# Optimization experiments

Hardware: AMD Instinct MI355X
Metric: run time of the kernel (lower is better)

## Reference

```python
import jax, jax.numpy as jnp
import numpy as np
import math

B, T, C, H = 8, 1024, 768, 12
HD = C // H  # 64


def setup_inputs() -> dict:
    key = jax.random.key(0)
    k1, k2, k3 = jax.random.split(key, 3)
    x = jax.random.normal(k1, (B, T, C), dtype=jnp.float32)
    W_attn = jax.random.normal(k2, (C, 3 * C), dtype=jnp.float32) * 0.02
    b_attn = jnp.zeros((3 * C,), dtype=jnp.float32)
    W_proj = jax.random.normal(k3, (C, C), dtype=jnp.float32) * (0.02 / math.sqrt(2 * 12))
    b_proj = jnp.zeros((C,), dtype=jnp.float32)
    return {"x": x, "W_attn": W_attn, "b_attn": b_attn, "W_proj": W_proj, "b_proj": b_proj}


def reference(x, W_attn, b_attn, W_proj, b_proj):
    Bx, Tx, Cx = x.shape
    qkv = x @ W_attn + b_attn                        # [B,T,3C]
    # faithful to original: reshape to (B,T,H,3*HD) then split last axis
    qkv = qkv.reshape(Bx, Tx, H, 3 * HD).transpose(0, 2, 1, 3)  # [B,H,T,3*HD]
    q, k, v = jnp.split(qkv, 3, axis=-1)             # each [B,H,T,HD]
    att = jnp.einsum('bhqd,bhkd->bhqk', q, k) / math.sqrt(HD)
    causal = jnp.tril(jnp.ones((Tx, Tx), dtype=bool))
    att = jnp.where(causal, att, -jnp.inf)
    att = jax.nn.softmax(att, axis=-1)
    y = jnp.einsum('bhqk,bhkd->bhqd', att, v)        # [B,H,T,HD]
    y = y.transpose(0, 2, 1, 3).reshape(Bx, Tx, Cx)  # [B,T,C]
    return y @ W_proj + b_proj
```

## Files before the change

### kernel.cpp

```cpp
#include <hip/hip_runtime.h>
#include <hip/hip_bf16.h>


#define TDIM 1024
#define CDIM 768
#define NDIM 2304

typedef __attribute__((ext_vector_type(8))) short bf16x8;
typedef __attribute__((ext_vector_type(8))) unsigned short u16x8;
typedef __attribute__((ext_vector_type(4))) float f32x4;

__device__ __forceinline__ unsigned short f2bf(float f) {
    unsigned int u;
    __builtin_memcpy(&u, &f, 4);
    u += 0x7FFFu + ((u >> 16) & 1u);
    return (unsigned short)(u >> 16);
}

__device__ __forceinline__ void async_copy16(void* lds, const void* g) {
    __builtin_amdgcn_global_load_lds(
        (const __attribute__((address_space(1))) void*)g,
        (__attribute__((address_space(3))) void*)lds, 16, 0, 0);
}

__global__ __launch_bounds__(256) void precast(
    const float* __restrict__ x, unsigned short* __restrict__ xb,
    const float* __restrict__ Wa, unsigned short* __restrict__ Wta,
    const float* __restrict__ Wp, unsigned short* __restrict__ Wtp)
{
    __shared__ float tile[32][33];
    int bid = blockIdx.x;
    const int tid = threadIdx.x;

    if (bid < 6144) {
        const size_t i = ((size_t)bid * 256 + tid) * 4;
        float4 v = *(const float4*)&x[i];
        ushort4 s;
        s.x = f2bf(v.x); s.y = f2bf(v.y); s.z = f2bf(v.z); s.w = f2bf(v.w);
        *(ushort4*)&xb[i] = s;
        return;
    }
    bid -= 6144;
    const float* W;
    unsigned short* Wt;
    int N, bx, by;
    if (bid < 1728) {
        W = Wa; Wt = Wta; N = NDIM; bx = bid % 72; by = bid / 72;
    } else {
        bid -= 1728;
        W = Wp; Wt = Wtp; N = CDIM; bx = bid % 24; by = bid / 24;
    }
    const int n0 = bx * 32;
    const int k0 = by * 32;
    const int tx = tid & 31;
    const int ty = tid >> 5;
#pragma unroll
    for (int i = 0; i < 4; ++i)
        tile[ty + i * 8][tx] = W[(size_t)(k0 + ty + i * 8) * N + n0 + tx];
    __syncthreads();
#pragma unroll
    for (int i = 0; i < 4; ++i)
        Wt[(size_t)(n0 + ty + i * 8) * CDIM + k0 + tx] = f2bf(tile[tx][ty + i * 8]);
}

__global__ __launch_bounds__(512, 4) void qkv_mfma(
    const unsigned short* __restrict__ xb, const unsigned short* __restrict__ Wt,
    const float* __restrict__ bias,
    unsigned short* __restrict__ Q, unsigned short* __restrict__ Kd,
    unsigned short* __restrict__ Vt)
{
    const int wg = ((int)blockIdx.x & 7) * 72 + ((int)blockIdx.x >> 3);
    const int bx = wg % 9;
    const int by = wg / 9;
    const int n0 = bx * 256;
    const int m0 = by * 128;
    const int tid = threadIdx.x;
    const int lane = tid & 63;
    const int w = tid >> 6;
    const int wm = w >> 2;
    const int wn = w & 3;
    const int lm = lane & 15;
    const int lq = lane >> 4;

    __shared__ __align__(16) unsigned short lds[36864];

    float bb[4];
#pragma unroll
    for (int ni = 0; ni < 4; ++ni) bb[ni] = bias[n0 + wn * 64 + ni * 16 + lm];

    f32x4 acc[4][4] = {};

    const int eo = lq ^ ((lm >> 1) & 3);
    int aoffc[4], boffc[4];
#pragma unroll
    for (int mi = 0; mi < 4; ++mi)
        aoffc[mi] = (wm * 64 + mi * 16 + lm) * 32 + eo * 8;
#pragma unroll
    for (int ni = 0; ni < 4; ++ni)
        boffc[ni] = 4096 + (wn * 64 + ni * 16 + lm) * 32 + eo * 8;

    const int rowA = tid >> 2;
    const int ccA = (tid & 3) ^ ((rowA >> 1) & 3);
    const int srcA = rowA * CDIM + ccA * 8;
    int srcB[2];
#pragma unroll
    for (int j = 0; j < 2; ++j) {
        const int lin = j * 512 + tid;
        const int rowB = lin >> 2;
        const int ccB = (lin & 3) ^ ((rowB >> 1) & 3);
        srcB[j] = rowB * CDIM + ccB * 8;
    }
    const unsigned short* xbb = xb + (size_t)m0 * CDIM;
    const unsigned short* Wtb = Wt + (size_t)n0 * CDIM;

#define STAGE(p, kt)                                                            \
    do {                                                                        \
        async_copy16(&lds[(p) * 12288 + w * 512], &xbb[srcA + (kt) * 32]);      \
        _Pragma("unroll")                                                       \
        for (int j = 0; j < 2; ++j)                                             \
            async_copy16(&lds[(p) * 12288 + 4096 + j * 4096 + w * 512],         \
                         &Wtb[srcB[j] + (kt) * 32]);                            \
    } while (0)

#define TILE(p, ktn)                                                            \
    do {                                                                        \
        STAGE((p + 2) % 3, ktn);                                                \
        bf16x8 a[4], b[4];                                                      \
        _Pragma("unroll")                                                       \
        for (int mi = 0; mi < 4; ++mi)                                          \
            a[mi] = *(const bf16x8*)&lds[(p) * 12288 + aoffc[mi]];              \
        _Pragma("unroll")                                                       \
        for (int ni = 0; ni < 4; ++ni)                                          \
            b[ni] = *(const bf16x8*)&lds[(p) * 12288 + boffc[ni]];              \
        __builtin_amdgcn_s_setprio(1);                                          \
        _Pragma("unroll")                                                       \
        for (int mi = 0; mi < 4; ++mi)                                          \
            _Pragma("unroll")                                                   \
            for (int ni = 0; ni < 4; ++ni)                                      \
                acc[mi][ni] = __builtin_amdgcn_mfma_f32_16x16x32_bf16(          \
                    a[mi], b[ni], acc[mi][ni], 0, 0, 0);                        \
        __builtin_amdgcn_s_setprio(0);                                          \
        asm volatile("s_waitcnt vmcnt(3)" ::: "memory");                        \
        __builtin_amdgcn_s_barrier();                                           \
    } while (0)

    STAGE(0, 0);
    STAGE(1, 1);
    asm volatile("s_waitcnt vmcnt(3)" ::: "memory");
    __builtin_amdgcn_s_barrier();

#pragma unroll 1
    for (int it = 0; it < 8; ++it) {
        const int k2 = (3 * it + 2 < 24) ? 3 * it + 2 : 23;
        const int k3 = (3 * it + 3 < 24) ? 3 * it + 3 : 23;
        const int k4 = (3 * it + 4 < 24) ? 3 * it + 4 : 23;
        TILE(0, k2);
        TILE(1, k3);
        TILE(2, k4);
    }

#undef STAGE
#undef TILE

    asm volatile("s_waitcnt vmcnt(0)" ::: "memory");
    __builtin_amdgcn_s_barrier();

    const int ga = bx * 4 + wn;
    const int which = ga % 3;
    const int h = ga / 3;

    if (which == 2) {
#pragma unroll
        for (int ni = 0; ni < 4; ++ni) {
            const int d = ni * 16 + lm;
#pragma unroll
            for (int mi = 0; mi < 4; ++mi) {
                const int gm0 = m0 + wm * 64 + mi * 16 + lq * 4;
                const int bidx = gm0 >> 10;
                const int t0 = gm0 & 1023;
                ushort4 sv;
                sv.x = f2bf(acc[mi][ni][0] + bb[ni]);
                sv.y = f2bf(acc[mi][ni][1] + bb[ni]);
                sv.z = f2bf(acc[mi][ni][2] + bb[ni]);
                sv.w = f2bf(acc[mi][ni][3] + bb[ni]);
                *(ushort4*)&Vt[(((size_t)bidx * 12 + h) * 64 + d) * TDIM + t0] = sv;
            }
        }
    } else {
        unsigned short* dst = (which == 0) ? Q : Kd;
        unsigned short* Es = &lds[w * 1152];
        const int erow = lane >> 2;
        const int ecol = lane & 3;
#pragma unroll
        for (int mi = 0; mi < 4; ++mi) {
#pragma unroll
            for (int r = 0; r < 4; ++r)
#pragma unroll
                for (int ni = 0; ni < 4; ++ni)
                    Es[(lq * 4 + r) * 72 + ni * 16 + lm] = f2bf(acc[mi][ni][r] + bb[ni]);
            const int t = m0 + wm * 64 + mi * 16 + erow;
            const int bidx = t >> 10;
            const int tt = t & 1023;
            unsigned short* drow = &dst[(((size_t)bidx * 12 + h) * TDIM + tt) * 64];
            u16x8 v0 = *(const u16x8*)&Es[erow * 72 + ecol * 16];
            u16x8 v1 = *(const u16x8*)&Es[erow * 72 + ecol * 16 + 8];
            *(u16x8*)&drow[ecol * 16] = v0;
            *(u16x8*)&drow[ecol * 16 + 8] = v1;
        }
    }
}

#define ATTN_TILE(aq, q0t, qt_t, l_p, o, ksb, vsb) do {                         \
    const bool diag_ = (kt == (qt_t));                                          \
    float pf[4][4];                                                             \
    _Pragma("unroll")                                                           \
    for (int nt = 0; nt < 4; ++nt) {                                            \
        f32x4 s = {};                                                           \
        _Pragma("unroll")                                                       \
        for (int kc = 0; kc < 2; ++kc) {                                        \
            bf16x8 bfrag = *(const bf16x8*)&(ksb)[(nt * 16 + lm) * 64 + cofs[kc]]; \
            s = __builtin_amdgcn_mfma_f32_16x16x32_bf16(aq[kc], bfrag, s, 0, 0, 0); \
        }                                                                       \
        const int keyg = kbase + nt * 16 + lm;                                  \
        _Pragma("unroll")                                                       \
        for (int r = 0; r < 4; ++r) {                                           \
            float p = __builtin_amdgcn_exp2f(s[r] * SC);                        \
            if (diag_) {                                                        \
                const int qg = (q0t) + w * 16 + lq * 4 + r;                     \
                if (keyg > qg) p = 0.f;                                         \
            }                                                                   \
            pf[nt][r] = p;                                                      \
        }                                                                       \
    }                                                                           \
    _Pragma("unroll")                                                           \
    for (int r = 0; r < 4; ++r) {                                               \
        l_p[r] += pf[0][r] + pf[1][r] + pf[2][r] + pf[3][r];                    \
        _Pragma("unroll")                                                       \
        for (int nt = 0; nt < 4; ++nt)                                          \
            Ps[w][lq * 4 + r][nt * 16 + lm] = f2bf(pf[nt][r]);                  \
    }                                                                           \
    {                                                                           \
        bf16x8 ap[2];                                                           \
        _Pragma("unroll")                                                       \
        for (int kc = 0; kc < 2; ++kc)                                          \
            ap[kc] = *(const bf16x8*)&Ps[w][lm][kc * 32 + lq * 8];              \
        _Pragma("unroll")                                                       \
        for (int nt = 0; nt < 4; ++nt) {                                        \
            _Pragma("unroll")                                                   \
            for (int kc = 0; kc < 2; ++kc) {                                    \
                bf16x8 bv = *(const bf16x8*)&(vsb)[(nt * 16 + lm) * 64 + cofs[kc]]; \
                o[nt] = __builtin_amdgcn_mfma_f32_16x16x32_bf16(ap[kc], bv, o[nt], 0, 0, 0); \
            }                                                                   \
        }                                                                       \
    }                                                                           \
} while (0)

#define ATTN_EPI(q0t, l_p, o) do {                                              \
    _Pragma("unroll")                                                           \
    for (int r = 0; r < 4; ++r) {                                               \
        float l = l_p[r];                                                       \
        _Pragma("unroll")                                                       \
        for (int off = 1; off < 16; off <<= 1) l += __shfl_xor(l, off);         \
        const float inv = 1.0f / l;                                             \
        const int qg = (q0t) + w * 16 + lq * 4 + r;                             \
        _Pragma("unroll")                                                       \
        for (int nt = 0; nt < 4; ++nt)                                          \
            Yb[(size_t)qg * 64 + nt * 16 + lm] = f2bf(o[nt][r] * inv);          \
    }                                                                           \
} while (0)

__global__ __launch_bounds__(256) void attn_mfma(
    const unsigned short* __restrict__ Q, const unsigned short* __restrict__ K,
    const unsigned short* __restrict__ Vt, unsigned short* __restrict__ Y)
{
    const int pi = blockIdx.x;
    const int bh = blockIdx.y;
    const int qtA = pi, qtB = 15 - pi;
    const int q0A = qtA * 64, q0B = qtB * 64;
    const int tid = threadIdx.x;
    const int lane = tid & 63;
    const int w = tid >> 6;
    const int lm = lane & 15;
    const int lq = lane >> 4;

    __shared__ __align__(16) unsigned short Ks2[2][4096];
    __shared__ __align__(16) unsigned short Vts2[2][4096];
    __shared__ __align__(16) unsigned short Ps[4][16][72];

    const unsigned short* Qb = Q + (size_t)bh * TDIM * 64;
    const unsigned short* Kb = K + (size_t)bh * TDIM * 64;
    const unsigned short* Vtb = Vt + (size_t)bh * 64 * TDIM;
    unsigned short* Yb = Y + (size_t)bh * TDIM * 64;

    bf16x8 aqA[2], aqB[2];
#pragma unroll
    for (int kc = 0; kc < 2; ++kc) {
        aqA[kc] = *(const bf16x8*)&Qb[(size_t)(q0A + w * 16 + lm) * 64 + kc * 32 + lq * 8];
        aqB[kc] = *(const bf16x8*)&Qb[(size_t)(q0B + w * 16 + lm) * 64 + kc * 32 + lq * 8];
    }

    int dstO[2], srcK[2], srcV[2];
#pragma unroll
    for (int it = 0; it < 2; ++it) {
        const int idx = it * 256 + tid;
        const int row = idx >> 3;
        const int cc = (idx & 7) ^ (row & 7);
        dstO[it] = idx * 8;
        srcK[it] = row * 64 + cc * 8;
        srcV[it] = row * TDIM + cc * 8;
    }
    int cofs[2];
#pragma unroll
    for (int kc = 0; kc < 2; ++kc)
        cofs[kc] = (((kc * 4 + lq) ^ (lm & 7)) * 8);

#define AST(bf, kb)                                                             \
    do {                                                                        \
        _Pragma("unroll")                                                       \
        for (int it = 0; it < 2; ++it) {                                        \
            async_copy16(&Ks2[bf][dstO[it]], &Kb[(size_t)(kb) * 64 + srcK[it]]); \
            async_copy16(&Vts2[bf][dstO[it]], &Vtb[(size_t)(kb) + srcV[it]]);   \
        }                                                                       \
    } while (0)

    float lA[4] = {}, lB[4] = {};
    f32x4 oA[4] = {}, oB[4] = {};

    const float SC = 0.125f * 1.44269504f;
    const int nktA = qtA + 1;
    const int nktB = qtB + 1;

    int buf = 0;
    AST(0, 0);
    asm volatile("s_waitcnt vmcnt(0)" ::: "memory");
    __builtin_amdgcn_s_barrier();

    for (int kt = 0; kt < nktB; ++kt) {
        const int kbase = kt * 64;
        if (kt + 1 < nktB) AST(buf ^ 1, kbase + 64);

        ATTN_TILE(aqB, q0B, qtB, lB, oB, Ks2[buf], Vts2[buf]);
        if (kt < nktA) ATTN_TILE(aqA, q0A, qtA, lA, oA, Ks2[buf], Vts2[buf]);

        asm volatile("s_waitcnt vmcnt(0)" ::: "memory");
        __builtin_amdgcn_s_barrier();
        buf ^= 1;
    }

#undef AST

    ATTN_EPI(q0A, lA, oA);
    ATTN_EPI(q0B, lB, oB);
}

__global__ __launch_bounds__(256, 3) void proj_mfma(
    const unsigned short* __restrict__ Y, const unsigned short* __restrict__ Wt,
    const float* __restrict__ bias, float* __restrict__ out)
{
    const int wg = ((int)blockIdx.x & 7) * 48 + ((int)blockIdx.x >> 3);
    const int bx = wg % 6;
    const int by = wg / 6;
    const int n0 = bx * 128;
    const int m0 = by * 128;
    const int tid = threadIdx.x;
    const int lane = tid & 63;
    const int w = tid >> 6;
    const int wm = w >> 1;
    const int wn = w & 1;
    const int lm = lane & 15;
    const int lq = lane >> 4;

    __shared__ __align__(16) unsigned short lds[24576];

    float bb[4];
#pragma unroll
    for (int ni = 0; ni < 4; ++ni) bb[ni] = bias[n0 + wn * 64 + ni * 16 + lm];

    f32x4 acc[4][4] = {};

    const int eo = lq ^ ((lm >> 1) & 3);
    int aoffc[4], boffc[4];
#pragma unroll
    for (int mi = 0; mi < 4; ++mi)
        aoffc[mi] = (wm * 64 + mi * 16 + lm) * 32 + eo * 8;
#pragma unroll
    for (int ni = 0; ni < 4; ++ni)
        boffc[ni] = 4096 + (wn * 64 + ni * 16 + lm) * 32 + eo * 8;

    size_t srcA[2];
    int srcB[2];
#pragma unroll
    for (int j = 0; j < 2; ++j) {
        const int lin = j * 256 + tid;
        const int row = lin >> 2;
        const int cc = (lin & 3) ^ ((row >> 1) & 3);
        const int m = m0 + row;
        srcA[j] = (size_t)(m >> 10) * 786432 + (size_t)(m & 1023) * 64 + cc * 8;
        srcB[j] = row * CDIM + cc * 8;
    }
    const unsigned short* Wtb = Wt + (size_t)n0 * CDIM;

#define PSTAGE(p, kt)                                                           \
    do {                                                                        \
        const int hof = ((kt) >> 1) * 65536 + ((kt) & 1) * 32;                  \
        _Pragma("unroll")                                                       \
        for (int j = 0; j < 2; ++j)                                             \
            async_copy16(&lds[(p) * 8192 + (j * 256 + tid) * 8],                \
                         &Y[srcA[j] + hof]);                                    \
        _Pragma("unroll")                                                       \
        for (int j = 0; j < 2; ++j)                                             \
            async_copy16(&lds[(p) * 8192 + 4096 + (j * 256 + tid) * 8],         \
                         &Wtb[srcB[j] + (kt) * 32]);                            \
    } while (0)

#define PTILE(p, ktn)                                                           \
    do {                                                                        \
        PSTAGE((p + 2) % 3, ktn);                                               \
        bf16x8 a[4], b[4];                                                      \
        _Pragma("unroll")                                                       \
        for (int mi = 0; mi < 4; ++mi)                                          \
            a[mi] = *(const bf16x8*)&lds[(p) * 8192 + aoffc[mi]];               \
        _Pragma("unroll")                                                       \
        for (int ni = 0; ni < 4; ++ni)                                          \
            b[ni] = *(const bf16x8*)&lds[(p) * 8192 + boffc[ni]];               \
        __builtin_amdgcn_s_setprio(1);                                          \
        _Pragma("unroll")                                                       \
        for (int mi = 0; mi < 4; ++mi)                                          \
            _Pragma("unroll")                                                   \
            for (int ni = 0; ni < 4; ++ni)                                      \
                acc[mi][ni] = __builtin_amdgcn_mfma_f32_16x16x32_bf16(          \
                    a[mi], b[ni], acc[mi][ni], 0, 0, 0);                        \
        __builtin_amdgcn_s_setprio(0);                                          \
        asm volatile("s_waitcnt vmcnt(4)" ::: "memory");                        \
        __builtin_amdgcn_s_barrier();                                           \
    } while (0)

    PSTAGE(0, 0);
    PSTAGE(1, 1);
    asm volatile("s_waitcnt vmcnt(4)" ::: "memory");
    __builtin_amdgcn_s_barrier();

#pragma unroll 1
    for (int it = 0; it < 8; ++it) {
        const int k2 = (3 * it + 2 < 24) ? 3 * it + 2 : 23;
        const int k3 = (3 * it + 3 < 24) ? 3 * it + 3 : 23;
        const int k4 = (3 * it + 4 < 24) ? 3 * it + 4 : 23;
        PTILE(0, k2);
        PTILE(1, k3);
        PTILE(2, k4);
    }

#undef PSTAGE
#undef PTILE

    asm volatile("s_waitcnt vmcnt(0)" ::: "memory");

#pragma unroll
    for (int ni = 0; ni < 4; ++ni) {
        const int gn = n0 + wn * 64 + ni * 16 + lm;
#pragma unroll
        for (int mi = 0; mi < 4; ++mi) {
#pragma unroll
            for (int r = 0; r < 4; ++r) {
                const int gm = m0 + wm * 64 + mi * 16 + lq * 4 + r;
                out[(size_t)gm * CDIM + gn] = acc[mi][ni][r] + bb[ni];
            }
        }
    }
}

extern "C" void kernel_launch(void* const* d_in, const int* in_sizes, int n_in,
                              void* d_out, int out_size, void* d_ws, size_t ws_size,
                              hipStream_t stream) {
    const float* x      = (const float*)d_in[0];
    const float* W_attn = (const float*)d_in[1];
    const float* b_attn = (const float*)d_in[2];
    const float* W_proj = (const float*)d_in[3];
    const float* b_proj = (const float*)d_in[4];
    float* out = (float*)d_out;

    const size_t per = (size_t)8 * 12 * 1024 * 64;
    unsigned short* Q   = (unsigned short*)d_ws;
    unsigned short* K   = Q + per;
    unsigned short* Vt  = K + per;
    unsigned short* xb  = Vt + per;
    unsigned short* Wta = xb + (size_t)8192 * CDIM;
    unsigned short* Wtp = Wta + (size_t)NDIM * CDIM;

    precast<<<dim3(8448), 256, 0, stream>>>(x, xb, W_attn, Wta, W_proj, Wtp);

    qkv_mfma<<<dim3(576), 512, 0, stream>>>(xb, Wta, b_attn, Q, K, Vt);
    attn_mfma<<<dim3(8, 96), 256, 0, stream>>>(Q, K, Vt, Q);
    proj_mfma<<<dim3(384), 256, 0, stream>>>(Q, Wtp, b_proj, out);
}
```

Measured before the change: 182.1 us.

## Load QKV GEMM weight fragments directly from global into registers, bypassing LDS

The QKV projection GEMM no longer stages the weight (B) tile through shared memory. Each wave now reads its B fragments straight from global memory into registers, and only the activation (A) tile stays in a triple-buffered LDS pipeline. This cuts LDS use per block from 72KB to 24KB, which can raise occupancy and removes the LDS reads for B. In exchange, B loads are issued just before the MFMAs, so their global/L2 latency is exposed; the two waves sharing a column read the same B twice; and the reads are strided across rows.

Result: slower. 223.9 us (+22.9%).

```diff
diff --git a/kernel.cpp b/kernel.cpp
--- a/kernel.cpp
+++ b/kernel.cpp
@@ -82,7 +82,7 @@
     const int lm = lane & 15;
     const int lq = lane >> 4;
 
-    __shared__ __align__(16) unsigned short lds[36864];
+    __shared__ __align__(16) unsigned short lds[12288];
 
     float bb[4];
 #pragma unroll
@@ -91,47 +91,31 @@
     f32x4 acc[4][4] = {};
 
     const int eo = lq ^ ((lm >> 1) & 3);
-    int aoffc[4], boffc[4];
+    int aoffc[4];
 #pragma unroll
     for (int mi = 0; mi < 4; ++mi)
         aoffc[mi] = (wm * 64 + mi * 16 + lm) * 32 + eo * 8;
-#pragma unroll
-    for (int ni = 0; ni < 4; ++ni)
-        boffc[ni] = 4096 + (wn * 64 + ni * 16 + lm) * 32 + eo * 8;
 
     const int rowA = tid >> 2;
     const int ccA = (tid & 3) ^ ((rowA >> 1) & 3);
     const int srcA = rowA * CDIM + ccA * 8;
-    int srcB[2];
-#pragma unroll
-    for (int j = 0; j < 2; ++j) {
-        const int lin = j * 512 + tid;
-        const int rowB = lin >> 2;
-        const int ccB = (lin & 3) ^ ((rowB >> 1) & 3);
-        srcB[j] = rowB * CDIM + ccB * 8;
-    }
     const unsigned short* xbb = xb + (size_t)m0 * CDIM;
-    const unsigned short* Wtb = Wt + (size_t)n0 * CDIM;
-
-#define STAGE(p, kt)                                                            \
+
+    const unsigned short* Bp = Wt + (size_t)(n0 + wn * 64 + lm) * CDIM + lq * 8;
+
+#define STAGE(p, kt) async_copy16(&lds[(p) * 4096 + tid * 8], &xbb[srcA + (kt) * 32])
+
+#define TILE(p, ktc, kts)                                                       \
     do {                                                                        \
-        async_copy16(&lds[(p) * 12288 + w * 512], &xbb[srcA + (kt) * 32]);      \
-        _Pragma("unroll")                                                       \
-        for (int j = 0; j < 2; ++j)                                             \
-            async_copy16(&lds[(p) * 12288 + 4096 + j * 4096 + w * 512],         \
-                         &Wtb[srcB[j] + (kt) * 32]);                            \
-    } while (0)
-
-#define TILE(p, ktn)                                                            \
-    do {                                                                        \
-        STAGE((p + 2) % 3, ktn);                                                \
-        bf16x8 a[4], b[4];                                                      \
+        bf16x8 b[4];                                                            \
+        _Pragma("unroll")                                                       \
+        for (int ni = 0; ni < 4; ++ni)                                          \
+            b[ni] = *(const bf16x8*)(Bp + ni * 16 * CDIM + (ktc) * 32);         \
+        STAGE((p + 2) % 3, kts);                                                \
+        bf16x8 a[4];                                                            \
         _Pragma("unroll")                                                       \
         for (int mi = 0; mi < 4; ++mi)                                          \
-            a[mi] = *(const bf16x8*)&lds[(p) * 12288 + aoffc[mi]];              \
-        _Pragma("unroll")                                                       \
-        for (int ni = 0; ni < 4; ++ni)                                          \
-            b[ni] = *(const bf16x8*)&lds[(p) * 12288 + boffc[ni]];              \
+            a[mi] = *(const bf16x8*)&lds[(p) * 4096 + aoffc[mi]];               \
         __builtin_amdgcn_s_setprio(1);                                          \
         _Pragma("unroll")                                                       \
         for (int mi = 0; mi < 4; ++mi)                                          \
@@ -140,23 +124,21 @@
                 acc[mi][ni] = __builtin_amdgcn_mfma_f32_16x16x32_bf16(          \
                     a[mi], b[ni], acc[mi][ni], 0, 0, 0);                        \
         __builtin_amdgcn_s_setprio(0);                                          \
-        asm volatile("s_waitcnt vmcnt(3)" ::: "memory");                        \
+        asm volatile("s_waitcnt vmcnt(1)" ::: "memory");                        \
         __builtin_amdgcn_s_barrier();                                           \
     } while (0)
 
     STAGE(0, 0);
     STAGE(1, 1);
-    asm volatile("s_waitcnt vmcnt(3)" ::: "memory");
+    asm volatile("s_waitcnt vmcnt(1)" ::: "memory");
     __builtin_amdgcn_s_barrier();
 
 #pragma unroll 1
     for (int it = 0; it < 8; ++it) {
-        const int k2 = (3 * it + 2 < 24) ? 3 * it + 2 : 23;
-        const int k3 = (3 * it + 3 < 24) ? 3 * it + 3 : 23;
-        const int k4 = (3 * it + 4 < 24) ? 3 * it + 4 : 23;
-        TILE(0, k2);
-        TILE(1, k3);
-        TILE(2, k4);
+        const int t0 = 3 * it;
+        TILE(0, t0,     (t0 + 2 < 24) ? t0 + 2 : 23);
+        TILE(1, t0 + 1, (t0 + 3 < 24) ? t0 + 3 : 23);
+        TILE(2, t0 + 2, (t0 + 4 < 24) ? t0 + 4 : 23);
     }
 
 #undef STAGE
```

## Interleave QK/softmax/PV phases of paired tiles and peel diagonal iterations

Applied to the files above, without the earlier changes.

Splits the attention tile into separate QK, softmax and PV stages and interleaves them across the two query tiles A and B, each with its own P buffer in LDS, so the MFMAs of one tile can overlap the exp and LDS work of the other. The key loop is also split into phases with compile-time flags, so causal masking code runs only on the diagonal iterations and the per-iteration `kt < nktA` check is removed. In exchange it doubles the P scratch in LDS and keeps more live score registers, which may add register pressure and lower occupancy.

After: 189.6 us. 4.1% more time.

```diff
diff --git a/kernel.cpp b/kernel.cpp
--- a/kernel.cpp
+++ b/kernel.cpp
@@ -210,9 +210,7 @@
     }
 }
 
-#define ATTN_TILE(aq, q0t, qt_t, l_p, o, ksb, vsb) do {                         \
-    const bool diag_ = (kt == (qt_t));                                          \
-    float pf[4][4];                                                             \
+#define QK_PART(sf, aq, ksb) do {                                               \
     _Pragma("unroll")                                                           \
     for (int nt = 0; nt < 4; ++nt) {                                            \
         f32x4 s = {};                                                           \
@@ -221,11 +219,19 @@
             bf16x8 bfrag = *(const bf16x8*)&(ksb)[(nt * 16 + lm) * 64 + cofs[kc]]; \
             s = __builtin_amdgcn_mfma_f32_16x16x32_bf16(aq[kc], bfrag, s, 0, 0, 0); \
         }                                                                       \
-        const int keyg = kbase + nt * 16 + lm;                                  \
+        sf[nt] = s;                                                             \
+    }                                                                           \
+} while (0)
+
+#define SM_PART(sf, l_p, ps, DIAG, q0t) do {                                    \
+    float pf[4][4];                                                             \
+    _Pragma("unroll")                                                           \
+    for (int nt = 0; nt < 4; ++nt) {                                            \
         _Pragma("unroll")                                                       \
         for (int r = 0; r < 4; ++r) {                                           \
-            float p = __builtin_amdgcn_exp2f(s[r] * SC);                        \
-            if (diag_) {                                                        \
+            float p = __builtin_amdgcn_exp2f(sf[nt][r] * SC);                   \
+            if (DIAG) {                                                         \
+                const int keyg = kbase + nt * 16 + lm;                          \
                 const int qg = (q0t) + w * 16 + lq * 4 + r;                     \
                 if (keyg > qg) p = 0.f;                                         \
             }                                                                   \
@@ -237,20 +243,21 @@
         l_p[r] += pf[0][r] + pf[1][r] + pf[2][r] + pf[3][r];                    \
         _Pragma("unroll")                                                       \
         for (int nt = 0; nt < 4; ++nt)                                          \
-            Ps[w][lq * 4 + r][nt * 16 + lm] = f2bf(pf[nt][r]);                  \
+            (ps)[(lq * 4 + r) * 72 + nt * 16 + lm] = f2bf(pf[nt][r]);           \
     }                                                                           \
-    {                                                                           \
-        bf16x8 ap[2];                                                           \
-        _Pragma("unroll")                                                       \
-        for (int kc = 0; kc < 2; ++kc)                                          \
-            ap[kc] = *(const bf16x8*)&Ps[w][lm][kc * 32 + lq * 8];              \
-        _Pragma("unroll")                                                       \
-        for (int nt = 0; nt < 4; ++nt) {                                        \
-            _Pragma("unroll")                                                   \
-            for (int kc = 0; kc < 2; ++kc) {                                    \
-                bf16x8 bv = *(const bf16x8*)&(vsb)[(nt * 16 + lm) * 64 + cofs[kc]]; \
-                o[nt] = __builtin_amdgcn_mfma_f32_16x16x32_bf16(ap[kc], bv, o[nt], 0, 0, 0); \
-            }                                                                   \
+} while (0)
+
+#define PV_PART(o, ps, vsb) do {                                                \
+    bf16x8 ap[2];                                                               \
+    _Pragma("unroll")                                                           \
+    for (int kc = 0; kc < 2; ++kc)                                              \
+        ap[kc] = *(const bf16x8*)&(ps)[lm * 72 + kc * 32 + lq * 8];             \
+    _Pragma("unroll")                                                           \
+    for (int nt = 0; nt < 4; ++nt) {                                            \
+        _Pragma("unroll")                                                       \
+        for (int kc = 0; kc < 2; ++kc) {                                        \
+            bf16x8 bv = *(const bf16x8*)&(vsb)[(nt * 16 + lm) * 64 + cofs[kc]]; \
+            o[nt] = __builtin_amdgcn_mfma_f32_16x16x32_bf16(ap[kc], bv, o[nt], 0, 0, 0); \
         }                                                                       \
     }                                                                           \
 } while (0)
@@ -285,7 +292,7 @@
 
     __shared__ __align__(16) unsigned short Ks2[2][4096];
     __shared__ __align__(16) unsigned short Vts2[2][4096];
-    __shared__ __align__(16) unsigned short Ps[4][16][72];
+    __shared__ __align__(16) unsigned short Ps[2][4][16 * 72];
 
     const unsigned short* Qb = Q + (size_t)bh * TDIM * 64;
     const unsigned short* Kb = K + (size_t)bh * TDIM * 64;
@@ -327,7 +334,6 @@
     f32x4 oA[4] = {}, oB[4] = {};
 
     const float SC = 0.125f * 1.44269504f;
-    const int nktA = qtA + 1;
     const int nktB = qtB + 1;
 
     int buf = 0;
@@ -335,18 +341,32 @@
     asm volatile("s_waitcnt vmcnt(0)" ::: "memory");
     __builtin_amdgcn_s_barrier();
 
-    for (int kt = 0; kt < nktB; ++kt) {
-        const int kbase = kt * 64;
-        if (kt + 1 < nktB) AST(buf ^ 1, kbase + 64);
-
-        ATTN_TILE(aqB, q0B, qtB, lB, oB, Ks2[buf], Vts2[buf]);
-        if (kt < nktA) ATTN_TILE(aqA, q0A, qtA, lA, oA, Ks2[buf], Vts2[buf]);
-
-        asm volatile("s_waitcnt vmcnt(0)" ::: "memory");
-        __builtin_amdgcn_s_barrier();
-        buf ^= 1;
-    }
-
+#define ITER(DO_A, DIAG_A, DIAG_B)                                              \
+    do {                                                                        \
+        const int kbase = kt * 64;                                              \
+        if (kt + 1 < nktB) AST(buf ^ 1, kbase + 64);                            \
+        f32x4 sB[4], sA[4];                                                     \
+        QK_PART(sB, aqB, Ks2[buf]);                                             \
+        if (DO_A) QK_PART(sA, aqA, Ks2[buf]);                                   \
+        SM_PART(sB, lB, &Ps[0][w][0], DIAG_B, q0B);                             \
+        if (DO_A) SM_PART(sA, lA, &Ps[1][w][0], DIAG_A, q0A);                   \
+        PV_PART(oB, &Ps[0][w][0], Vts2[buf]);                                   \
+        if (DO_A) PV_PART(oA, &Ps[1][w][0], Vts2[buf]);                         \
+        asm volatile("s_waitcnt vmcnt(0)" ::: "memory");                        \
+        __builtin_amdgcn_s_barrier();                                           \
+        buf ^= 1;                                                               \
+    } while (0)
+
+    int kt = 0;
+#pragma unroll 1
+    for (; kt < qtA; ++kt) ITER(true, false, false);
+    ITER(true, true, false);
+    ++kt;
+#pragma unroll 1
+    for (; kt < qtB; ++kt) ITER(false, false, false);
+    ITER(false, false, true);
+
+#undef ITER
 #undef AST
 
     ATTN_EPI(q0A, lA, oA);
```
